# Kernel optimization log

Hardware: AMD Instinct MI355X
Metric: run time of the kernel (lower is better)

## Reference

```python
import jax, jax.numpy as jnp
import numpy as np

B, S, HID = 1, 2048, 1024
NH, NKV, HD = 16, 4, 64
SCALING = 0.125  # attention_multiplier = 1/sqrt(head_dim)
ROPE_THETA = 10000.0
NEG_MIN = jnp.finfo(jnp.float32).min


def rotate_half(x):
    x1, x2 = jnp.split(x, 2, axis=-1)
    return jnp.concatenate([-x2, x1], axis=-1)


def setup_inputs() -> dict:
    key = jax.random.key(0)
    ks = jax.random.split(key, 6)
    hidden_states = jax.random.normal(ks[0], (B, S, HID), dtype=jnp.float32)
    # RoPE tables: [1, 1, S, HD]
    inv_freq = 1.0 / (ROPE_THETA ** (np.arange(0, HD, 2, dtype=np.float32) / HD))
    t = np.arange(S, dtype=np.float32)
    freqs = np.outer(t, inv_freq)                      # [S, HD/2]
    emb = np.concatenate([freqs, freqs], axis=-1)      # [S, HD]
    cos = jnp.asarray(np.cos(emb))[None, None]
    sin = jnp.asarray(np.sin(emb))[None, None]
    attention_mask = jnp.ones((B, S), dtype=bool)
    sc = 0.02
    Wq = jax.random.normal(ks[1], (HID, NH * HD), dtype=jnp.float32) * sc
    Wk = jax.random.normal(ks[2], (HID, NKV * HD), dtype=jnp.float32) * sc
    Wv = jax.random.normal(ks[3], (HID, NKV * HD), dtype=jnp.float32) * sc
    Wo = jax.random.normal(ks[4], (NH * HD, HID), dtype=jnp.float32) * sc
    return {"hidden_states": hidden_states, "cos": cos, "sin": sin,
            "attention_mask": attention_mask, "Wq": Wq, "Wk": Wk, "Wv": Wv, "Wo": Wo}


def reference(hidden_states, cos, sin, attention_mask, Wq, Wk, Wv, Wo):
    b, s, _ = hidden_states.shape
    # projections -> [B, H, S, D]
    q = (hidden_states @ Wq).reshape(b, s, NH, HD).transpose(0, 2, 1, 3)
    k = (hidden_states @ Wk).reshape(b, s, NKV, HD).transpose(0, 2, 1, 3)
    v = (hidden_states @ Wv).reshape(b, s, NKV, HD).transpose(0, 2, 1, 3)
    # RoPE (full head_dim rotation; cos/sin broadcast over batch/heads)
    q = q * cos + rotate_half(q) * sin
    k = k * cos + rotate_half(k) * sin
    # repeat_kv: expand kv heads to match query heads
    n_rep = NH // NKV
    k = jnp.repeat(k, n_rep, axis=1)
    v = jnp.repeat(v, n_rep, axis=1)
    # scores: [B, H, Sq, Sk]
    attn = jnp.einsum('bhqd,bhkd->bhqk', q, k) * SCALING
    mask = attention_mask[:, None, None, :].astype(attn.dtype)  # bool padding mask
    attn = attn + (1.0 - mask) * NEG_MIN
    attn = jax.nn.softmax(attn.astype(jnp.float32), axis=-1).astype(q.dtype)
    out = jnp.einsum('bhqk,bhkd->bhqd', attn, v)
    out = out.transpose(0, 2, 1, 3).reshape(b, s, NH * HD)
    return out @ Wo
```

## Files before the change

### kernel.cpp

```cpp
#include <hip/hip_runtime.h>
#include <stdint.h>

typedef __attribute__((ext_vector_type(8))) short short8;
typedef __attribute__((ext_vector_type(4))) short short4v;
typedef __attribute__((ext_vector_type(4))) float floatx4;
typedef __attribute__((ext_vector_type(16))) float floatx16;
typedef __attribute__((ext_vector_type(2))) unsigned int uint2v;
typedef __attribute__((ext_vector_type(4))) unsigned int uint4v;

#define AS1 __attribute__((address_space(1)))
#define AS3 __attribute__((address_space(3)))

__device__ __forceinline__ void async16(const void* g, void* l) {
  __builtin_amdgcn_global_load_lds((const AS1 unsigned int*)g, (AS3 unsigned int*)l, 16, 0, 0);
}

__device__ __forceinline__ short f2bf(float f) {
  unsigned u = __float_as_uint(f);
  u = (u + 0x7FFF + ((u >> 16) & 1)) >> 16;
  return (short)u;
}

__device__ __forceinline__ short f2h(float f) {
  _Float16 h = (_Float16)f;
  return *(short*)&h;
}
__device__ __forceinline__ float h2f(short s) {
  _Float16 h = *(_Float16*)&s;
  return (float)h;
}

#if __has_builtin(__builtin_amdgcn_cvt_pk_bf16_f32)
typedef __bf16 bf16x2 __attribute__((ext_vector_type(2)));
__device__ __forceinline__ unsigned pack2(float lo, float hi) {
  bf16x2 t = __builtin_amdgcn_cvt_pk_bf16_f32(lo, hi);
  return *(unsigned*)&t;
}
#else
__device__ __forceinline__ unsigned pack2(float lo, float hi) {
  return __builtin_amdgcn_perm(__float_as_uint(hi) + 0x8000u,
                               __float_as_uint(lo) + 0x8000u, 0x07060302u);
}
#endif

__device__ __forceinline__ uint2v permswap32(unsigned a, unsigned b) {
#if __has_builtin(__builtin_amdgcn_permlane32_swap)
  return __builtin_amdgcn_permlane32_swap(a, b, false, false);
#else
  asm volatile("v_permlane32_swap_b32 %0, %1" : "+v"(a), "+v"(b));
  uint2v r; r.x = a; r.y = b; return r;
#endif
}

__device__ __forceinline__ void stage_sw(const short* src, int stride,
                                         short* tile, int cb, int lane) {
  int i = cb + lane;
  int r = i >> 3, j = i & 7;
  async16(src + (size_t)r * stride + ((j ^ (r & 7)) * 8), tile + cb * 8);
}
__device__ __forceinline__ int sw(int row, int c8) {
  return row * 64 + ((c8 ^ (row & 7)) * 8);
}

__global__ void k_prep(const float* __restrict__ X, const float* __restrict__ Wq,
                       const float* __restrict__ Wk, const float* __restrict__ Wv,
                       const float* __restrict__ Wo, short* __restrict__ Xb,
                       short* __restrict__ Wqkvt, short* __restrict__ Wot) {
  int b = blockIdx.x, tid = threadIdx.x;
  if (b < 2048) {
    int i = b * 1024 + tid * 4;
    floatx4 v = *(const floatx4*)(X + i);
    short4v o;
    o.x = f2bf(v.x); o.y = f2bf(v.y); o.z = f2bf(v.z); o.w = f2bf(v.w);
    *(short4v*)(Xb + i) = o;
    return;
  }
  const float* src; short* dst; int N, brel, rowoff;
  if (b < 3072)      { src = Wq; dst = Wqkvt; N = 1024; brel = b - 2048; rowoff = 0; }
  else if (b < 3328) { src = Wk; dst = Wqkvt; N = 256;  brel = b - 3072; rowoff = 1024; }
  else if (b < 3584) { src = Wv; dst = Wqkvt; N = 256;  brel = b - 3328; rowoff = 1280; }
  else               { src = Wo; dst = Wot;   N = 1024; brel = b - 3584; rowoff = 0; }
  __shared__ short t[32][33];
  int nt = N >> 5;
  int n0 = (brel % nt) * 32, k0 = (brel / nt) * 32;
  int tx = tid & 31, ty = tid >> 5;
#pragma unroll
  for (int i = 0; i < 4; i++)
    t[ty + 8 * i][tx] = f2bf(src[(size_t)(k0 + ty + 8 * i) * N + n0 + tx]);
  __syncthreads();
#pragma unroll
  for (int i = 0; i < 4; i++)
    dst[(size_t)(rowoff + n0 + ty + 8 * i) * 1024 + k0 + tx] = t[tx][ty + 8 * i];
}

__global__ __launch_bounds__(256) void k_gemmqkv(const short* __restrict__ A,
                                                 const short* __restrict__ Bt,
                                                 short* __restrict__ Qb,
                                                 short* __restrict__ Kb,
                                                 short* __restrict__ Vtb,
                                                 const float* __restrict__ cosp,
                                                 const float* __restrict__ sinp,
                                                 float qscale) {
  int tid = threadIdx.x;
  int flat = blockIdx.y * 24 + blockIdx.x;
  int swz = (flat & 7) * 96 + (flat >> 3);
  int bx = swz % 24, by = swz / 24;
  int w = tid >> 6, lane = tid & 63, quad = lane >> 4, l16 = lane & 15;
  __shared__ short As[2][4096];
  __shared__ short Bs[2][4096];
  const int K = 1024;
  const short* Ag = A + (size_t)(by * 64) * K;
  const short* Bg = Bt + (size_t)(bx * 64) * K;
  floatx4 acc[4] = {};
#pragma unroll
  for (int t = 0; t < 2; t++) stage_sw(Ag, K, As[0], (w * 2 + t) * 64, lane);
#pragma unroll
  for (int t = 0; t < 2; t++) stage_sw(Bg, K, Bs[0], (w * 2 + t) * 64, lane);
  for (int kt = 0; kt < 16; kt++) {
    __syncthreads();
    int cur = kt & 1, nxt = cur ^ 1;
    if (kt + 1 < 16) {
#pragma unroll
      for (int t = 0; t < 2; t++) stage_sw(Ag + (kt + 1) * 64, K, As[nxt], (w * 2 + t) * 64, lane);
#pragma unroll
      for (int t = 0; t < 2; t++) stage_sw(Bg + (kt + 1) * 64, K, Bs[nxt], (w * 2 + t) * 64, lane);
    }
#pragma unroll
    for (int ks = 0; ks < 2; ks++) {
      short8 af = *(const short8*)&As[cur][sw(w * 16 + l16, ks * 4 + quad)];
#pragma unroll
      for (int j = 0; j < 4; j++) {
        short8 bfr = *(const short8*)&Bs[cur][sw(j * 16 + l16, ks * 4 + quad)];
        acc[j] = __builtin_amdgcn_mfma_f32_16x16x32_bf16(af, bfr, acc[j], 0, 0, 0);
      }
    }
  }
  if (bx < 20) {
    short* dst; float scale;
    if (bx < 16) { dst = Qb + (size_t)bx * 2048 * 64; scale = qscale; }
    else         { dst = Kb + (size_t)(bx - 16) * 2048 * 64; scale = 1.0f; }
#pragma unroll
    for (int r = 0; r < 4; r++) {
      int s = by * 64 + w * 16 + quad * 4 + r;
#pragma unroll
      for (int j = 0; j < 2; j++) {
        int d = j * 16 + l16;
        float c = cosp[s * 64 + d], sn = sinp[s * 64 + d];
        float v0 = acc[j][r], v1 = acc[j + 2][r];
        dst[(size_t)s * 64 + d]      = f2bf((v0 * c - v1 * sn) * scale);
        dst[(size_t)s * 64 + 32 + d] = f2bf((v1 * c + v0 * sn) * scale);
      }
    }
  } else {
    short* dst = Vtb + (size_t)(bx - 20) * 64 * 2048;
#pragma unroll
    for (int j = 0; j < 4; j++) {
      int d = j * 16 + l16;
      short4v pk;
#pragma unroll
      for (int r = 0; r < 4; r++) pk[r] = f2bf(acc[j][r]);
      *(short4v*)&dst[(size_t)d * 2048 + by * 64 + w * 16 + quad * 4] = pk;
    }
  }
}

__global__ __launch_bounds__(256) void k_gemm(const short* __restrict__ A,
                                              const short* __restrict__ Bt,
                                              float* __restrict__ C,
                                              int M, int N, int K) {
  int tid = threadIdx.x;
  int flat = blockIdx.y * 16 + blockIdx.x;
  int swz = (flat & 7) * 64 + (flat >> 3);
  int bx = swz & 15, by = swz >> 4;
  int w = tid >> 6, lane = tid & 63, quad = lane >> 4, l16 = lane & 15;
  __shared__ short As[2][4096];
  __shared__ short Bs[2][4096];
  const short* Ag = A + (size_t)(by * 64) * K;
  const short* Bg = Bt + (size_t)(bx * 64) * K;
  floatx4 acc[4] = {};
  int kiters = K >> 6;
#pragma unroll
  for (int t = 0; t < 2; t++) stage_sw(Ag, K, As[0], (w * 2 + t) * 64, lane);
#pragma unroll
  for (int t = 0; t < 2; t++) stage_sw(Bg, K, Bs[0], (w * 2 + t) * 64, lane);
  for (int kt = 0; kt < kiters; kt++) {
    __syncthreads();
    int cur = kt & 1, nxt = cur ^ 1;
    if (kt + 1 < kiters) {
#pragma unroll
      for (int t = 0; t < 2; t++) stage_sw(Ag + (kt + 1) * 64, K, As[nxt], (w * 2 + t) * 64, lane);
#pragma unroll
      for (int t = 0; t < 2; t++) stage_sw(Bg + (kt + 1) * 64, K, Bs[nxt], (w * 2 + t) * 64, lane);
    }
#pragma unroll
    for (int ks = 0; ks < 2; ks++) {
      short8 af = *(const short8*)&As[cur][sw(w * 16 + l16, ks * 4 + quad)];
#pragma unroll
      for (int j = 0; j < 4; j++) {
        short8 bfr = *(const short8*)&Bs[cur][sw(j * 16 + l16, ks * 4 + quad)];
        acc[j] = __builtin_amdgcn_mfma_f32_16x16x32_bf16(af, bfr, acc[j], 0, 0, 0);
      }
    }
  }
#pragma unroll
  for (int j = 0; j < 4; j++)
#pragma unroll
    for (int r = 0; r < 4; r++) {
      int row = by * 64 + w * 16 + quad * 4 + r;
      int col = bx * 64 + j * 16 + l16;
      __builtin_nontemporal_store(acc[j][r], &C[(size_t)row * N + col]);
    }
}

__global__ __launch_bounds__(256, 4) void k_attn(const short* __restrict__ Qb,
                                                 const short* __restrict__ Kb,
                                                 const short* __restrict__ Vt,
                                                 short* __restrict__ Opart,
                                                 float* __restrict__ lpart) {
  int flat = (blockIdx.z * 16 + blockIdx.y) * 16 + blockIdx.x;
  int swz = (flat & 7) * 128 + (flat >> 3);
  int qt = swz & 15;
  int h = (swz >> 4) & 15;
  int sp = swz >> 8;
  int kvh = h >> 2;
  int tid = threadIdx.x, w = tid >> 6, lane = tid & 63;
  int l32 = lane & 31, hi = lane >> 5;
  __shared__ short Ks[2][4096];
  __shared__ short Vs[2][4096];
  const short* Qg = Qb + ((size_t)h * 2048 + qt * 128 + w * 32) * 64;
  const short* Kg0 = Kb + ((size_t)kvh * 2048 + sp * 512) * 64;
  const short* Vg0 = Vt + (size_t)kvh * 64 * 2048 + sp * 512;
  short8 qf[4];
#pragma unroll
  for (int ks4 = 0; ks4 < 4; ks4++)
    qf[ks4] = *(const short8*)(Qg + l32 * 64 + ks4 * 16 + hi * 8);
#pragma unroll
  for (int t = 0; t < 2; t++) stage_sw(Kg0, 64, Ks[0], (w * 2 + t) * 64, lane);
#pragma unroll
  for (int t = 0; t < 2; t++) stage_sw(Vg0, 2048, Vs[0], (w * 2 + t) * 64, lane);
  short8 vones;
  {
    short one = (short)0x3F80;
#pragma unroll
    for (int j = 0; j < 8; j++) vones[j] = (l32 == 0) ? one : (short)0;
  }
  floatx16 accO[2] = {};
  floatx16 accL = {};
  for (int kt = 0; kt < 8; kt++) {
    __syncthreads();
    if (kt + 1 < 8) {
      int nb = (kt + 1) & 1;
#pragma unroll
      for (int t = 0; t < 2; t++)
        stage_sw(Kg0 + (kt + 1) * 4096, 64, Ks[nb], (w * 2 + t) * 64, lane);
#pragma unroll
      for (int t = 0; t < 2; t++)
        stage_sw(Vg0 + (kt + 1) * 64, 2048, Vs[nb], (w * 2 + t) * 64, lane);
    }
    int cu = kt & 1;
#pragma unroll
    for (int kb = 0; kb < 2; kb++) {
      floatx16 accS = {};
#pragma unroll
      for (int ks4 = 0; ks4 < 4; ks4++) {
        short8 af = *(const short8*)&Ks[cu][sw(kb * 32 + l32, ks4 * 2 + hi)];
        accS = __builtin_amdgcn_mfma_f32_32x32x16_bf16(af, qf[ks4], accS, 0, 0, 0);
      }
#pragma unroll
      for (int c = 0; c < 2; c++) {
        float p0 = __builtin_amdgcn_exp2f(accS[8 * c + 0]);
        float p1 = __builtin_amdgcn_exp2f(accS[8 * c + 1]);
        float p2 = __builtin_amdgcn_exp2f(accS[8 * c + 2]);
        float p3 = __builtin_amdgcn_exp2f(accS[8 * c + 3]);
        float p4 = __builtin_amdgcn_exp2f(accS[8 * c + 4]);
        float p5 = __builtin_amdgcn_exp2f(accS[8 * c + 5]);
        float p6 = __builtin_amdgcn_exp2f(accS[8 * c + 6]);
        float p7 = __builtin_amdgcn_exp2f(accS[8 * c + 7]);
        uint2v r0 = permswap32(pack2(p0, p1), pack2(p4, p5));
        uint2v r1 = permswap32(pack2(p2, p3), pack2(p6, p7));
        uint4v pw; pw.x = r0.x; pw.y = r1.x; pw.z = r0.y; pw.w = r1.y;
        short8 pa = *(short8*)&pw;
        int kstep = kb * 2 + c;
        accL = __builtin_amdgcn_mfma_f32_32x32x16_bf16(pa, vones, accL, 0, 0, 0);
#pragma unroll
        for (int db = 0; db < 2; db++) {
          short8 vf = *(const short8*)&Vs[cu][sw(db * 32 + l32, kstep * 2 + hi)];
          accO[db] = __builtin_amdgcn_mfma_f32_32x32x16_bf16(pa, vf, accO[db], 0, 0, 0);
        }
      }
    }
  }
  if (l32 == 0) {
#pragma unroll
    for (int reg = 0; reg < 16; reg++) {
      int q = (reg & 3) + 8 * (reg >> 2) + 4 * hi;
      __builtin_nontemporal_store(accL[reg],
          &lpart[(size_t)sp * 16 * 2048 + h * 2048 + qt * 128 + w * 32 + q]);
    }
  }
  short* Op = Opart + (size_t)sp * 2048 * 1024;
#pragma unroll
  for (int db = 0; db < 2; db++)
#pragma unroll
    for (int reg = 0; reg < 16; reg++) {
      int q = (reg & 3) + 8 * (reg >> 2) + 4 * hi;
      int srow = qt * 128 + w * 32 + q;
      int col = h * 64 + db * 32 + l32;
      __builtin_nontemporal_store(f2h(accO[db][reg]), &Op[(size_t)srow * 1024 + col]);
    }
}

__global__ void k_comb(const short* __restrict__ Opart, const float* __restrict__ lpart,
                       short* __restrict__ AOb) {
  int idx = (blockIdx.x * 256 + threadIdx.x) * 4;
  int s = idx >> 10, h = (idx & 1023) >> 6;
  float l = 0.f;
#pragma unroll
  for (int sp = 0; sp < 4; sp++)
    l += __builtin_nontemporal_load(&lpart[sp * 16 * 2048 + h * 2048 + s]);
  float inv = 1.0f / l;
  float a0 = 0.f, a1 = 0.f, a2 = 0.f, a3 = 0.f;
#pragma unroll
  for (int sp = 0; sp < 4; sp++) {
    short4v hv = __builtin_nontemporal_load(
        (const short4v*)(Opart + (size_t)sp * 2048 * 1024 + idx));
    a0 += h2f(hv.x); a1 += h2f(hv.y); a2 += h2f(hv.z); a3 += h2f(hv.w);
  }
  uint2v pk;
  pk.x = pack2(a0 * inv, a1 * inv);
  pk.y = pack2(a2 * inv, a3 * inv);
  *(uint2v*)&AOb[idx] = pk;
}

extern "C" void kernel_launch(void* const* d_in, const int* in_sizes, int n_in,
                              void* d_out, int out_size, void* d_ws, size_t ws_size,
                              hipStream_t stream) {
  const float* X    = (const float*)d_in[0];
  const float* cosp = (const float*)d_in[1];
  const float* sinp = (const float*)d_in[2];
  const float* Wq = (const float*)d_in[4];
  const float* Wk = (const float*)d_in[5];
  const float* Wv = (const float*)d_in[6];
  const float* Wo = (const float*)d_in[7];
  float* out = (float*)d_out;

  short* Xb    = (short*)d_ws;
  short* Wqkvt = Xb + 2097152;
  short* Wot   = Wqkvt + 1572864;
  short* Qb2   = Wot + 1048576;
  short* Kb2   = Qb2 + 2097152;
  short* Vtb   = Kb2 + 524288;
  short* AOb   = Vtb + 524288;
  short* Opart = AOb + 2097152;
  float* lpart = (float*)(Opart + 4 * 2097152);

  const float QSCALE = 0.125f * 1.44269504088896340736f;

  k_prep<<<4608, 256, 0, stream>>>(X, Wq, Wk, Wv, Wo, Xb, Wqkvt, Wot);
  k_gemmqkv<<<dim3(24, 32), 256, 0, stream>>>(Xb, Wqkvt, Qb2, Kb2, Vtb, cosp, sinp, QSCALE);
  k_attn<<<dim3(16, 16, 4), 256, 0, stream>>>(Qb2, Kb2, Vtb, Opart, lpart);
  k_comb<<<2048, 256, 0, stream>>>(Opart, lpart, AOb);
  k_gemm<<<dim3(16, 32), 256, 0, stream>>>(AOb, Wot, out, 2048, 1024, 1024);
}
```

Before: 136.7 us.

## Fuse split-KV combine into output projection GEMM A-tile staging

Removes the separate combine kernel and the AOb intermediate buffer. The output-projection GEMM now loads the four fp16 partial attention outputs directly, sums them, normalizes by the reciprocal of the summed row denominators (precomputed into shared memory), and writes bf16 A tiles into swizzled LDS, prefetching the next k-slice into registers. The attention kernel's partial stores are switched from nontemporal to regular so they may stay in cache for the fused consumer. The trade-off is that each of the 16 column-tile blocks re-reads and re-reduces the same partials, multiplying partial-read traffic, and register-based A staging replaces async loads.

```diff
diff --git a/kernel.cpp b/kernel.cpp
--- a/kernel.cpp
+++ b/kernel.cpp
@@ -164,54 +164,6 @@
   }
 }
 
-__global__ __launch_bounds__(256) void k_gemm(const short* __restrict__ A,
-                                              const short* __restrict__ Bt,
-                                              float* __restrict__ C,
-                                              int M, int N, int K) {
-  int tid = threadIdx.x;
-  int flat = blockIdx.y * 16 + blockIdx.x;
-  int swz = (flat & 7) * 64 + (flat >> 3);
-  int bx = swz & 15, by = swz >> 4;
-  int w = tid >> 6, lane = tid & 63, quad = lane >> 4, l16 = lane & 15;
-  __shared__ short As[2][4096];
-  __shared__ short Bs[2][4096];
-  const short* Ag = A + (size_t)(by * 64) * K;
-  const short* Bg = Bt + (size_t)(bx * 64) * K;
-  floatx4 acc[4] = {};
-  int kiters = K >> 6;
-#pragma unroll
-  for (int t = 0; t < 2; t++) stage_sw(Ag, K, As[0], (w * 2 + t) * 64, lane);
-#pragma unroll
-  for (int t = 0; t < 2; t++) stage_sw(Bg, K, Bs[0], (w * 2 + t) * 64, lane);
-  for (int kt = 0; kt < kiters; kt++) {
-    __syncthreads();
-    int cur = kt & 1, nxt = cur ^ 1;
-    if (kt + 1 < kiters) {
-#pragma unroll
-      for (int t = 0; t < 2; t++) stage_sw(Ag + (kt + 1) * 64, K, As[nxt], (w * 2 + t) * 64, lane);
-#pragma unroll
-      for (int t = 0; t < 2; t++) stage_sw(Bg + (kt + 1) * 64, K, Bs[nxt], (w * 2 + t) * 64, lane);
-    }
-#pragma unroll
-    for (int ks = 0; ks < 2; ks++) {
-      short8 af = *(const short8*)&As[cur][sw(w * 16 + l16, ks * 4 + quad)];
-#pragma unroll
-      for (int j = 0; j < 4; j++) {
-        short8 bfr = *(const short8*)&Bs[cur][sw(j * 16 + l16, ks * 4 + quad)];
-        acc[j] = __builtin_amdgcn_mfma_f32_16x16x32_bf16(af, bfr, acc[j], 0, 0, 0);
-      }
-    }
-  }
-#pragma unroll
-  for (int j = 0; j < 4; j++)
-#pragma unroll
-    for (int r = 0; r < 4; r++) {
-      int row = by * 64 + w * 16 + quad * 4 + r;
-      int col = bx * 64 + j * 16 + l16;
-      __builtin_nontemporal_store(acc[j][r], &C[(size_t)row * N + col]);
-    }
-}
-
 __global__ __launch_bounds__(256, 4) void k_attn(const short* __restrict__ Qb,
                                                  const short* __restrict__ Kb,
                                                  const short* __restrict__ Vt,
@@ -294,8 +246,7 @@
 #pragma unroll
     for (int reg = 0; reg < 16; reg++) {
       int q = (reg & 3) + 8 * (reg >> 2) + 4 * hi;
-      __builtin_nontemporal_store(accL[reg],
-          &lpart[(size_t)sp * 16 * 2048 + h * 2048 + qt * 128 + w * 32 + q]);
+      lpart[(size_t)sp * 16 * 2048 + h * 2048 + qt * 128 + w * 32 + q] = accL[reg];
     }
   }
   short* Op = Opart + (size_t)sp * 2048 * 1024;
@@ -306,30 +257,124 @@
       int q = (reg & 3) + 8 * (reg >> 2) + 4 * hi;
       int srow = qt * 128 + w * 32 + q;
       int col = h * 64 + db * 32 + l32;
-      __builtin_nontemporal_store(f2h(accO[db][reg]), &Op[(size_t)srow * 1024 + col]);
-    }
-}
-
-__global__ void k_comb(const short* __restrict__ Opart, const float* __restrict__ lpart,
-                       short* __restrict__ AOb) {
-  int idx = (blockIdx.x * 256 + threadIdx.x) * 4;
-  int s = idx >> 10, h = (idx & 1023) >> 6;
-  float l = 0.f;
-#pragma unroll
-  for (int sp = 0; sp < 4; sp++)
-    l += __builtin_nontemporal_load(&lpart[sp * 16 * 2048 + h * 2048 + s]);
-  float inv = 1.0f / l;
-  float a0 = 0.f, a1 = 0.f, a2 = 0.f, a3 = 0.f;
+      Op[(size_t)srow * 1024 + col] = f2h(accO[db][reg]);
+    }
+}
+
+__global__ __launch_bounds__(256) void k_gemmo(const short* __restrict__ Opart,
+                                               const float* __restrict__ lpart,
+                                               const short* __restrict__ Bt,
+                                               float* __restrict__ C) {
+  int tid = threadIdx.x;
+  int flat = blockIdx.y * 16 + blockIdx.x;
+  int swz = (flat & 7) * 64 + (flat >> 3);
+  int bx = swz & 15, by = swz >> 4;
+  int w = tid >> 6, lane = tid & 63, quad = lane >> 4, l16 = lane & 15;
+  __shared__ short As[2][4096];
+  __shared__ short Bs[2][4096];
+  __shared__ float invt[1024];
+  const short* Bg = Bt + (size_t)(bx * 64) * 1024;
+  {
+    int idx = tid * 4;
+#pragma unroll
+    for (int e = 0; e < 4; e++) {
+      int r = (idx + e) >> 4, h = (idx + e) & 15;
+      float l = 0.f;
+#pragma unroll
+      for (int sp = 0; sp < 4; sp++)
+        l += lpart[sp * 16 * 2048 + h * 2048 + by * 64 + r];
+      invt[idx + e] = 1.0f / l;
+    }
+  }
+  int i0 = (w * 2) * 64 + lane, i1 = (w * 2 + 1) * 64 + lane;
+  int r0 = i0 >> 3, jj0 = (i0 & 7) ^ (r0 & 7);
+  int r1 = i1 >> 3, jj1 = (i1 & 7) ^ (r1 & 7);
+  const short* Abase0 = Opart + (size_t)(by * 64 + r0) * 1024 + jj0 * 8;
+  const short* Abase1 = Opart + (size_t)(by * 64 + r1) * 1024 + jj1 * 8;
+  __syncthreads();
+  short8 hv0[4], hv1[4];
 #pragma unroll
   for (int sp = 0; sp < 4; sp++) {
-    short4v hv = __builtin_nontemporal_load(
-        (const short4v*)(Opart + (size_t)sp * 2048 * 1024 + idx));
-    a0 += h2f(hv.x); a1 += h2f(hv.y); a2 += h2f(hv.z); a3 += h2f(hv.w);
-  }
-  uint2v pk;
-  pk.x = pack2(a0 * inv, a1 * inv);
-  pk.y = pack2(a2 * inv, a3 * inv);
-  *(uint2v*)&AOb[idx] = pk;
+    hv0[sp] = *(const short8*)(Abase0 + (size_t)sp * 2097152);
+    hv1[sp] = *(const short8*)(Abase1 + (size_t)sp * 2097152);
+  }
+  {
+    float iv0 = invt[r0 * 16 + 0], iv1 = invt[r1 * 16 + 0];
+    uint4v pw;
+    pw.x = pack2((h2f(hv0[0][0]) + h2f(hv0[1][0]) + h2f(hv0[2][0]) + h2f(hv0[3][0])) * iv0,
+                 (h2f(hv0[0][1]) + h2f(hv0[1][1]) + h2f(hv0[2][1]) + h2f(hv0[3][1])) * iv0);
+    pw.y = pack2((h2f(hv0[0][2]) + h2f(hv0[1][2]) + h2f(hv0[2][2]) + h2f(hv0[3][2])) * iv0,
+                 (h2f(hv0[0][3]) + h2f(hv0[1][3]) + h2f(hv0[2][3]) + h2f(hv0[3][3])) * iv0);
+    pw.z = pack2((h2f(hv0[0][4]) + h2f(hv0[1][4]) + h2f(hv0[2][4]) + h2f(hv0[3][4])) * iv0,
+                 (h2f(hv0[0][5]) + h2f(hv0[1][5]) + h2f(hv0[2][5]) + h2f(hv0[3][5])) * iv0);
+    pw.w = pack2((h2f(hv0[0][6]) + h2f(hv0[1][6]) + h2f(hv0[2][6]) + h2f(hv0[3][6])) * iv0,
+                 (h2f(hv0[0][7]) + h2f(hv0[1][7]) + h2f(hv0[2][7]) + h2f(hv0[3][7])) * iv0);
+    *(uint4v*)&As[0][i0 * 8] = pw;
+    pw.x = pack2((h2f(hv1[0][0]) + h2f(hv1[1][0]) + h2f(hv1[2][0]) + h2f(hv1[3][0])) * iv1,
+                 (h2f(hv1[0][1]) + h2f(hv1[1][1]) + h2f(hv1[2][1]) + h2f(hv1[3][1])) * iv1);
+    pw.y = pack2((h2f(hv1[0][2]) + h2f(hv1[1][2]) + h2f(hv1[2][2]) + h2f(hv1[3][2])) * iv1,
+                 (h2f(hv1[0][3]) + h2f(hv1[1][3]) + h2f(hv1[2][3]) + h2f(hv1[3][3])) * iv1);
+    pw.z = pack2((h2f(hv1[0][4]) + h2f(hv1[1][4]) + h2f(hv1[2][4]) + h2f(hv1[3][4])) * iv1,
+                 (h2f(hv1[0][5]) + h2f(hv1[1][5]) + h2f(hv1[2][5]) + h2f(hv1[3][5])) * iv1);
+    pw.w = pack2((h2f(hv1[0][6]) + h2f(hv1[1][6]) + h2f(hv1[2][6]) + h2f(hv1[3][6])) * iv1,
+                 (h2f(hv1[0][7]) + h2f(hv1[1][7]) + h2f(hv1[2][7]) + h2f(hv1[3][7])) * iv1);
+    *(uint4v*)&As[0][i1 * 8] = pw;
+  }
+#pragma unroll
+  for (int t = 0; t < 2; t++) stage_sw(Bg, 1024, Bs[0], (w * 2 + t) * 64, lane);
+  floatx4 acc[4] = {};
+  for (int kt = 0; kt < 16; kt++) {
+    __syncthreads();
+    int cur = kt & 1, nxt = cur ^ 1;
+    if (kt + 1 < 16) {
+#pragma unroll
+      for (int sp = 0; sp < 4; sp++) {
+        hv0[sp] = *(const short8*)(Abase0 + (size_t)sp * 2097152 + (kt + 1) * 64);
+        hv1[sp] = *(const short8*)(Abase1 + (size_t)sp * 2097152 + (kt + 1) * 64);
+      }
+#pragma unroll
+      for (int t = 0; t < 2; t++) stage_sw(Bg + (kt + 1) * 64, 1024, Bs[nxt], (w * 2 + t) * 64, lane);
+    }
+#pragma unroll
+    for (int ks = 0; ks < 2; ks++) {
+      short8 af = *(const short8*)&As[cur][sw(w * 16 + l16, ks * 4 + quad)];
+#pragma unroll
+      for (int j = 0; j < 4; j++) {
+        short8 bfr = *(const short8*)&Bs[cur][sw(j * 16 + l16, ks * 4 + quad)];
+        acc[j] = __builtin_amdgcn_mfma_f32_16x16x32_bf16(af, bfr, acc[j], 0, 0, 0);
+      }
+    }
+    if (kt + 1 < 16) {
+      float iv0 = invt[r0 * 16 + (kt + 1)], iv1 = invt[r1 * 16 + (kt + 1)];
+      uint4v pw;
+      pw.x = pack2((h2f(hv0[0][0]) + h2f(hv0[1][0]) + h2f(hv0[2][0]) + h2f(hv0[3][0])) * iv0,
+                   (h2f(hv0[0][1]) + h2f(hv0[1][1]) + h2f(hv0[2][1]) + h2f(hv0[3][1])) * iv0);
+      pw.y = pack2((h2f(hv0[0][2]) + h2f(hv0[1][2]) + h2f(hv0[2][2]) + h2f(hv0[3][2])) * iv0,
+                   (h2f(hv0[0][3]) + h2f(hv0[1][3]) + h2f(hv0[2][3]) + h2f(hv0[3][3])) * iv0);
+      pw.z = pack2((h2f(hv0[0][4]) + h2f(hv0[1][4]) + h2f(hv0[2][4]) + h2f(hv0[3][4])) * iv0,
+                   (h2f(hv0[0][5]) + h2f(hv0[1][5]) + h2f(hv0[2][5]) + h2f(hv0[3][5])) * iv0);
+      pw.w = pack2((h2f(hv0[0][6]) + h2f(hv0[1][6]) + h2f(hv0[2][6]) + h2f(hv0[3][6])) * iv0,
+                   (h2f(hv0[0][7]) + h2f(hv0[1][7]) + h2f(hv0[2][7]) + h2f(hv0[3][7])) * iv0);
+      *(uint4v*)&As[nxt][i0 * 8] = pw;
+      pw.x = pack2((h2f(hv1[0][0]) + h2f(hv1[1][0]) + h2f(hv1[2][0]) + h2f(hv1[3][0])) * iv1,
+                   (h2f(hv1[0][1]) + h2f(hv1[1][1]) + h2f(hv1[2][1]) + h2f(hv1[3][1])) * iv1);
+      pw.y = pack2((h2f(hv1[0][2]) + h2f(hv1[1][2]) + h2f(hv1[2][2]) + h2f(hv1[3][2])) * iv1,
+                   (h2f(hv1[0][3]) + h2f(hv1[1][3]) + h2f(hv1[2][3]) + h2f(hv1[3][3])) * iv1);
+      pw.z = pack2((h2f(hv1[0][4]) + h2f(hv1[1][4]) + h2f(hv1[2][4]) + h2f(hv1[3][4])) * iv1,
+                   (h2f(hv1[0][5]) + h2f(hv1[1][5]) + h2f(hv1[2][5]) + h2f(hv1[3][5])) * iv1);
+      pw.w = pack2((h2f(hv1[0][6]) + h2f(hv1[1][6]) + h2f(hv1[2][6]) + h2f(hv1[3][6])) * iv1,
+                   (h2f(hv1[0][7]) + h2f(hv1[1][7]) + h2f(hv1[2][7]) + h2f(hv1[3][7])) * iv1);
+      *(uint4v*)&As[nxt][i1 * 8] = pw;
+    }
+  }
+#pragma unroll
+  for (int j = 0; j < 4; j++)
+#pragma unroll
+    for (int r = 0; r < 4; r++) {
+      int row = by * 64 + w * 16 + quad * 4 + r;
+      int col = bx * 64 + j * 16 + l16;
+      __builtin_nontemporal_store(acc[j][r], &C[(size_t)row * 1024 + col]);
+    }
 }
 
 extern "C" void kernel_launch(void* const* d_in, const int* in_sizes, int n_in,
@@ -350,8 +395,7 @@
   short* Qb2   = Wot + 1048576;
   short* Kb2   = Qb2 + 2097152;
   short* Vtb   = Kb2 + 524288;
-  short* AOb   = Vtb + 524288;
-  short* Opart = AOb + 2097152;
+  short* Opart = Vtb + 524288;
   float* lpart = (float*)(Opart + 4 * 2097152);
 
   const float QSCALE = 0.125f * 1.44269504088896340736f;
@@ -359,6 +403,5 @@
   k_prep<<<4608, 256, 0, stream>>>(X, Wq, Wk, Wv, Wo, Xb, Wqkvt, Wot);
   k_gemmqkv<<<dim3(24, 32), 256, 0, stream>>>(Xb, Wqkvt, Qb2, Kb2, Vtb, cosp, sinp, QSCALE);
   k_attn<<<dim3(16, 16, 4), 256, 0, stream>>>(Qb2, Kb2, Vtb, Opart, lpart);
-  k_comb<<<2048, 256, 0, stream>>>(Opart, lpart, AOb);
-  k_gemm<<<dim3(16, 32), 256, 0, stream>>>(AOb, Wot, out, 2048, 1024, 1024);
-}
+  k_gemmo<<<dim3(16, 32), 256, 0, stream>>>(Opart, lpart, Wot, out);
+}
```

New measurement: 144.5 us. +5.7%, slower.
